# Optimization experiments

Hardware: AMD Instinct MI355X
Metric: run time of the kernel (lower is better)

Reference implementation:

```python
import jax, jax.numpy as jnp
import numpy as np

# Model config (matches init_kwargs)
L_F, DELTA_F, L_S, DELTA_S = 1, 1, 32, 16
HIDDEN = 32       # SSM state dim H
GRU_H = 64        # slow-branch GRU hidden
N_GRU = 4
B, T = 4, 32768


def setup_inputs() -> dict:
    key = jax.random.key(0)
    ks = jax.random.split(key, 13)
    def nrm(k, shape, s=0.05):
        return jax.random.normal(k, shape, dtype=jnp.float32) * s
    return {
        "x": jax.random.normal(ks[0], (B, T), dtype=jnp.float32),
        # SlowBranch params
        "fc_in_w": nrm(ks[1], (GRU_H, 1), 0.3),
        "fc_in_b": nrm(ks[2], (GRU_H,)),
        "gru_wih": nrm(ks[3], (N_GRU, 3 * GRU_H, GRU_H), 0.1),
        "gru_whh": nrm(ks[4], (N_GRU, 3 * GRU_H, GRU_H), 0.1),
        "gru_bih": nrm(ks[5], (N_GRU, 3 * GRU_H)),
        "gru_bhh": nrm(ks[6], (N_GRU, 3 * GRU_H)),
        "out_fc_w": nrm(ks[7], (2 * HIDDEN, GRU_H), 0.1),
        "out_fc_b": nrm(ks[8], (2 * HIDDEN,)),
        # Fast branch params (F_IN: 1->H, F_OUT: H->1)
        "fin_w": nrm(ks[9], (HIDDEN, 1), 0.3),
        "fin_b": nrm(ks[10], (HIDDEN,)),
        "fout_w": nrm(ks[11], (1, HIDDEN), 0.1),
        "fout_b": nrm(ks[12], (1,)),
    }


def _gru_layer(xs, Wih, Whh, bih, bhh):
    """Torch-convention GRU layer. xs: (N, L, H_in) -> (N, L, H)."""
    H = Whh.shape[1]
    # Precompute input-side gate pre-activations: (N, L, 3H)
    xp = jnp.einsum('nlh,gh->nlg', xs, Wih) + bih
    def step(h, xt):
        gh = h @ Whh.T + bhh                       # (N, 3H)
        ir, iz, inew = jnp.split(xt, 3, axis=-1)
        hr, hz, hnew = jnp.split(gh, 3, axis=-1)
        r = jax.nn.sigmoid(ir + hr)
        z = jax.nn.sigmoid(iz + hz)
        n = jnp.tanh(inew + r * hnew)
        h = (1.0 - z) * n + z * h
        return h, h
    h0 = jnp.zeros((xs.shape[0], H), xs.dtype)
    _, ys = jax.lax.scan(step, h0, jnp.swapaxes(xp, 0, 1))  # (L, N, H)
    return jnp.swapaxes(ys, 0, 1)


def reference(x, fc_in_w, fc_in_b, gru_wih, gru_whh, gru_bih, gru_bhh,
              out_fc_w, out_fc_b, fin_w, fin_b, fout_w, fout_b):
    Bsz, Tlen = x.shape
    num_slow = (Tlen - L_S) // DELTA_S + 1

    frame_idx = jnp.arange(num_slow)[:, None] * DELTA_S + jnp.arange(L_S)[None, :]
    x_s = x[:, frame_idx].reshape(Bsz * num_slow, L_S, 1)      # (N, L_s, 1)
    h = jax.nn.relu(x_s * fc_in_w[:, 0] + fc_in_b)             # (N, L_s, GRU_H)
    for l in range(gru_wih.shape[0]):
        h = _gru_layer(h, gru_wih[l], gru_whh[l], gru_bih[l], gru_bhh[l])
    eps = h[:, -1, :] @ out_fc_w.T + out_fc_b                  # (N, 2H)
    eps = eps.reshape(Bsz, num_slow, 2 * HIDDEN)
    A_slow = jax.nn.sigmoid(eps[..., :HIDDEN])                 # (B, S, H)
    g_slow = eps[..., HIDDEN:]                                 # (B, S, H)

    # ---- Fast branch: per-sample diagonal linear SSM scan ----
    delta = DELTA_S // DELTA_F
    idx = jnp.clip(jnp.arange(Tlen) // delta - 1, 0, num_slow - 1)  # (T,)
    A_t = A_slow[:, idx, :]                                    # (B, T, H)
    u_t = (x[..., None] * fin_w[:, 0] + fin_b) * g_slow[:, idx, :]  # (B, T, H)

    def step(hc, inp):
        A, u = inp
        hn = A * hc + u
        return hn, hn
    h0 = jnp.zeros((Bsz, HIDDEN), x.dtype)
    _, h_all = jax.lax.scan(step, h0,
                            (jnp.swapaxes(A_t, 0, 1), jnp.swapaxes(u_t, 0, 1)))
    # h_all: (T, B, H); F_OUT applied to every state
    return jnp.einsum('tbh,h->bt', h_all, fout_w[0]) + fout_b[0]   # (B, T)
```

## Files before the change

kernel.cpp:

```cpp
#include <hip/hip_runtime.h>
#include <hip/hip_bf16.h>

typedef __bf16 bf16x8 __attribute__((ext_vector_type(8)));
typedef short short8 __attribute__((ext_vector_type(8)));
typedef float f32x4 __attribute__((ext_vector_type(4)));
typedef unsigned short ushort_t;

#define T_LEN 32768
#define B_SZ 4
#define NSLOW 2047
#define NSEQ (B_SZ * NSLOW)
#define GH 64
#define G3 192
#define NL 4
#define HID 32
#define NCH 256
#define L2E 1.44269504088896341f

#define OFF_X    0
#define OFF_FCW  131072
#define OFF_FCB  131136
#define OFF_WIH  131200
#define OFF_WHH  180352
#define OFF_BIH  229504
#define OFF_BHH  230272
#define OFF_OFW  231040
#define OFF_OFB  235136
#define OFF_FINW 235200
#define OFF_FINB 235232
#define OFF_FOW  235264
#define OFF_FOB  235296
#define CONV_TOTAL 235297
#define CONV_PAD_BYTES 470656

static __device__ __forceinline__ float bf2f(ushort_t u) {
    union { unsigned u; float f; } c; c.u = ((unsigned)u) << 16; return c.f;
}
static __device__ __forceinline__ ushort_t f2bf(float f) {
    union { float f; unsigned u; } c; c.f = f;
    unsigned r = (c.u + 0x7FFFu + ((c.u >> 16) & 1u)) >> 16;
    return (ushort_t)r;
}
static __device__ __forceinline__ unsigned pk2bf(float a, float b) {
    float2 f; f.x = a; f.y = b;
    __hip_bfloat162 h = __float22bfloat162_rn(f);
    unsigned u;
    __builtin_memcpy(&u, &h, 4);
    return u;
}
static __device__ __forceinline__ f32x4 mfma16(short8 a, short8 b, f32x4 c) {
    return __builtin_amdgcn_mfma_f32_16x16x32_bf16(
        __builtin_bit_cast(bf16x8, a), __builtin_bit_cast(bf16x8, b), c, 0, 0, 0);
}
static __device__ __forceinline__ int xoff(int t, int kb, int seq) {
    return ((((t << 3) + kb) << 4) + (seq ^ (kb & 7))) << 3;
}
static __device__ __forceinline__ short8 load_frag_scaled(const ushort_t* p, float s) {
    uint4 r = *(const uint4*)p;
    unsigned aa[4] = {r.x, r.y, r.z, r.w};
    short8 o;
#pragma unroll
    for (int i = 0; i < 4; ++i) {
        o[2 * i]     = (short)f2bf(bf2f((ushort_t)(aa[i] & 0xffffu)) * s);
        o[2 * i + 1] = (short)f2bf(bf2f((ushort_t)(aa[i] >> 16)) * s);
    }
    return o;
}

struct Ptrs13 { const void* p[13]; };

__global__ __launch_bounds__(256) void convert_kernel(Ptrs13 ptrs,
                                                      int* __restrict__ flag,
                                                      ushort_t* __restrict__ dst)
{
    __shared__ int scnt;
    if (threadIdx.x == 0) scnt = 0;
    __syncthreads();
    {
        ushort_t u = ((const ushort_t*)ptrs.p[0])[threadIdx.x];
        int e = (u >> 7) & 0xFF;
        int ok = (e >= 80 && e <= 141) ? 1 : 0;
#pragma unroll
        for (int d = 1; d < 64; d <<= 1) ok += __shfl_xor(ok, d, 64);
        if ((threadIdx.x & 63) == 0) atomicAdd(&scnt, ok);
    }
    __syncthreads();
    const bool isbf = (scnt >= 224);
    if (blockIdx.x == 0 && threadIdx.x == 0) *flag = isbf ? 1 : 0;

    const int offs[14] = {OFF_X, OFF_FCW, OFF_FCB, OFF_WIH, OFF_WHH, OFF_BIH,
                          OFF_BHH, OFF_OFW, OFF_OFB, OFF_FINW, OFF_FINB,
                          OFF_FOW, OFF_FOB, CONV_TOTAL};
    for (int idx = blockIdx.x * 256 + threadIdx.x; idx < CONV_TOTAL;
         idx += gridDim.x * 256) {
        int s = 0;
#pragma unroll
        for (int j = 1; j < 13; ++j) if (idx >= offs[j]) s = j;
        int k = idx - offs[s];
        ushort_t v = isbf ? ((const ushort_t*)ptrs.p[s])[k]
                          : f2bf(((const float*)ptrs.p[s])[k]);
        dst[idx] = v;
    }
}

__global__ __launch_bounds__(256, 2) void gru_kernel(
    const ushort_t* __restrict__ x, const ushort_t* __restrict__ fcw,
    const ushort_t* __restrict__ fcb, const ushort_t* __restrict__ wih,
    const ushort_t* __restrict__ whh, const ushort_t* __restrict__ bih,
    const ushort_t* __restrict__ bhh, const ushort_t* __restrict__ ofw,
    const ushort_t* __restrict__ ofb, float* __restrict__ Aslow,
    float* __restrict__ gslow)
{
    __shared__ short8 Xs8[4096];
    short* Xs = (short*)Xs8;
    const int tid = threadIdx.x;
    const int w = tid >> 6, lane = tid & 63;
    const int q = lane >> 4, m = lane & 15;
    const int jb = w * 16;
    const int n0 = blockIdx.x * 16;

#pragma unroll 1
    for (int ii = 0; ii < 16; ++ii) {
        int cid = ii * 256 + tid;
        int seq = cid & 15, kb = (cid >> 4) & 7, t = cid >> 7;
        int n = n0 + seq; if (n > NSEQ - 1) n = NSEQ - 1;
        int b = n / NSLOW, s = n - b * NSLOW;
        float xv = bf2f(x[b * T_LEN + s * 16 + t]);
        short8 v;
#pragma unroll
        for (int i = 0; i < 8; ++i) {
            int g = kb * 8 + i;
            float h = fmaf(xv, bf2f(fcw[g]), bf2f(fcb[g]));
            h = h > 0.f ? h : 0.f;
            v[i] = (short)f2bf(h);
        }
        Xs8[xoff(t, kb, seq) >> 3] = v;
    }

    const int col0 = jb + 4 * q;
    const int kbw = (col0 >> 3);
    const int wsub = (col0 & 7);
    const int kofs = q * 8;
    const int wbase0 = ((kbw << 4) + (m ^ (kbw & 7))) * 8 + wsub;

    float hc[4];
#pragma unroll 1
    for (int l = 0; l < NL; ++l) {
        const ushort_t* wl = wih + l * G3 * GH;
        const ushort_t* ul = whh + l * G3 * GH;
        short8 wR0 = load_frag_scaled(wl + (0 * 64 + jb + m) * 64 + kofs, -L2E);
        short8 wR1 = load_frag_scaled(wl + (0 * 64 + jb + m) * 64 + 32 + kofs, -L2E);
        short8 wZ0 = load_frag_scaled(wl + (1 * 64 + jb + m) * 64 + kofs, -L2E);
        short8 wZ1 = load_frag_scaled(wl + (1 * 64 + jb + m) * 64 + 32 + kofs, -L2E);
        short8 wN0 = load_frag_scaled(wl + (2 * 64 + jb + m) * 64 + kofs, 2.f * L2E);
        short8 wN1 = load_frag_scaled(wl + (2 * 64 + jb + m) * 64 + 32 + kofs, 2.f * L2E);
        short8 uR0 = load_frag_scaled(ul + (0 * 64 + jb + m) * 64 + kofs, -L2E);
        short8 uR1 = load_frag_scaled(ul + (0 * 64 + jb + m) * 64 + 32 + kofs, -L2E);
        short8 uZ0 = load_frag_scaled(ul + (1 * 64 + jb + m) * 64 + kofs, -L2E);
        short8 uZ1 = load_frag_scaled(ul + (1 * 64 + jb + m) * 64 + 32 + kofs, -L2E);
        short8 uN0 = load_frag_scaled(ul + (2 * 64 + jb + m) * 64 + kofs, 2.f * L2E);
        short8 uN1 = load_frag_scaled(ul + (2 * 64 + jb + m) * 64 + 32 + kofs, 2.f * L2E);

        f32x4 bRv, bZv, bNXv, bNHv;
#pragma unroll
        for (int i = 0; i < 4; ++i) {
            int c = col0 + i;
            bRv[i]  = -L2E * (bf2f(bih[l * G3 + c]) + bf2f(bhh[l * G3 + c]));
            bZv[i]  = -L2E * (bf2f(bih[l * G3 + 64 + c]) + bf2f(bhh[l * G3 + 64 + c]));
            bNXv[i] = 2.f * L2E * bf2f(bih[l * G3 + 128 + c]);
            bNHv[i] = 2.f * L2E * bf2f(bhh[l * G3 + 128 + c]);
        }

        hc[0] = hc[1] = hc[2] = hc[3] = 0.f;

        __syncthreads();
        int iA = xoff(0, q, m) >> 3;
        int iB = xoff(0, 4 + q, m) >> 3;
        int wb = wbase0;

        short8 cx0 = Xs8[iA], cx1 = Xs8[iB];
        short8 nx0 = Xs8[iA + 128], nx1 = Xs8[iB + 128];
        f32x4 xR = bRv, xZ = bZv, xN = bNXv;
        xR = mfma16(wR0, cx0, xR); xR = mfma16(wR1, cx1, xR);
        xZ = mfma16(wZ0, cx0, xZ); xZ = mfma16(wZ1, cx1, xZ);
        xN = mfma16(wN0, cx0, xN); xN = mfma16(wN1, cx1, xN);
#pragma unroll
        for (int i = 0; i < 4; ++i) {
            float r = __builtin_amdgcn_rcpf(1.f + __builtin_amdgcn_exp2f(xR[i]));
            float z = __builtin_amdgcn_rcpf(1.f + __builtin_amdgcn_exp2f(xZ[i]));
            float yp = fmaf(r, bNHv[i], xN[i]);
            float nn = fmaf(-2.f,
                __builtin_amdgcn_rcpf(1.f + __builtin_amdgcn_exp2f(yp)), 1.f);
            hc[i] = fmaf(z, hc[i] - nn, nn);
        }
        *(uint2*)(Xs + wb) = make_uint2(pk2bf(hc[0], hc[1]), pk2bf(hc[2], hc[3]));
        xR = bRv; xZ = bZv; xN = bNXv;
        xR = mfma16(wR0, nx0, xR); xR = mfma16(wR1, nx1, xR);
        xZ = mfma16(wZ0, nx0, xZ); xZ = mfma16(wZ1, nx1, xZ);
        xN = mfma16(wN0, nx0, xN); xN = mfma16(wN1, nx1, xN);
        iA += 128; iB += 128; wb += 1024;

#pragma unroll 1
        for (int t = 1; t < 32; ++t) {
            __syncthreads();
            short8 bh0 = Xs8[iA - 128];
            short8 bh1 = Xs8[iB - 128];
            short8 px0, px1;
            if (t < 31) {
                px0 = Xs8[iA + 128];
                px1 = Xs8[iB + 128];
            }
            f32x4 aR = xR, aZ = xZ, aNH = bNHv;
            aR  = mfma16(uR0, bh0, aR);  aR  = mfma16(uR1, bh1, aR);
            aZ  = mfma16(uZ0, bh0, aZ);  aZ  = mfma16(uZ1, bh1, aZ);
            aNH = mfma16(uN0, bh0, aNH); aNH = mfma16(uN1, bh1, aNH);
#pragma unroll
            for (int i = 0; i < 4; ++i) {
                float r = __builtin_amdgcn_rcpf(1.f + __builtin_amdgcn_exp2f(aR[i]));
                float z = __builtin_amdgcn_rcpf(1.f + __builtin_amdgcn_exp2f(aZ[i]));
                float yp = fmaf(r, aNH[i], xN[i]);
                float nn = fmaf(-2.f,
                    __builtin_amdgcn_rcpf(1.f + __builtin_amdgcn_exp2f(yp)), 1.f);
                hc[i] = fmaf(z, hc[i] - nn, nn);
            }
            *(uint2*)(Xs + wb) =
                make_uint2(pk2bf(hc[0], hc[1]), pk2bf(hc[2], hc[3]));
            if (t < 31) {
                xR = bRv; xZ = bZv; xN = bNXv;
                xR = mfma16(wR0, px0, xR); xR = mfma16(wR1, px1, xR);
                xZ = mfma16(wZ0, px0, xZ); xZ = mfma16(wZ1, px1, xZ);
                xN = mfma16(wN0, px0, xN); xN = mfma16(wN1, px1, xN);
            }
            iA += 128; iB += 128; wb += 1024;
        }
    }

    __syncthreads();
    short8 aL0 = Xs8[xoff(31, q, m) >> 3];
    short8 aL1 = Xs8[xoff(31, 4 + q, m) >> 3];
    float sc = (w < 2) ? -L2E : 1.f;
    short8 o0 = load_frag_scaled(ofw + (jb + m) * 64 + kofs, sc);
    short8 o1 = load_frag_scaled(ofw + (jb + m) * 64 + 32 + kofs, sc);
    f32x4 aE = {bf2f(ofb[col0]) * sc, bf2f(ofb[col0 + 1]) * sc,
                bf2f(ofb[col0 + 2]) * sc, bf2f(ofb[col0 + 3]) * sc};
    aE = mfma16(o0, aL0, aE);
    aE = mfma16(o1, aL1, aE);
    int n = n0 + m;
    if (w < 2) {
        f32x4 v;
#pragma unroll
        for (int i = 0; i < 4; ++i)
            v[i] = __builtin_amdgcn_rcpf(1.f + __builtin_amdgcn_exp2f(aE[i]));
        *(f32x4*)(Aslow + n * HID + col0) = v;
    } else {
        *(f32x4*)(gslow + n * HID + (col0 - 32)) = aE;
    }
}

__global__ __launch_bounds__(256) void pass1_kernel(
    const ushort_t* __restrict__ x, const float* __restrict__ Aslow,
    const float* __restrict__ gslow, const ushort_t* __restrict__ finw,
    const ushort_t* __restrict__ finb, float* __restrict__ P,
    float* __restrict__ S)
{
    int gt = blockIdx.x * 256 + threadIdx.x;
    int h = gt & 31, c = (gt >> 5) & 255, b = gt >> 13;
    float fw = bf2f(finw[h]), fb = bf2f(finb[h]);
    float Pv = 1.f, Sv = 0.f;
    int t0 = c * 128;
#pragma unroll 1
    for (int seg = 0; seg < 8; ++seg) {
        int sidx = (t0 >> 4) + seg - 1;
        if (sidx < 0) sidx = 0;
        if (sidx > NSLOW - 1) sidx = NSLOW - 1;
        float A = Aslow[(b * NSLOW + sidx) * HID + h];
        float g = gslow[(b * NSLOW + sidx) * HID + h];
        float fwg = fw * g, fbg = fb * g;
        const uint4* px = (const uint4*)(x + b * T_LEN + t0 + seg * 16);
        uint4 ra = px[0], rb = px[1];
        unsigned xa[8] = {ra.x, ra.y, ra.z, ra.w, rb.x, rb.y, rb.z, rb.w};
#pragma unroll
        for (int j = 0; j < 8; ++j) {
            float x0 = bf2f((ushort_t)(xa[j] & 0xffffu));
            float x1 = bf2f((ushort_t)(xa[j] >> 16));
            Sv = fmaf(A, Sv, fmaf(x0, fwg, fbg));
            Sv = fmaf(A, Sv, fmaf(x1, fwg, fbg));
        }
        float A2 = A * A, A4 = A2 * A2, A8 = A4 * A4;
        Pv *= A8 * A8;
    }
    P[(b * HID + h) * NCH + c] = Pv;
    S[(b * HID + h) * NCH + c] = Sv;
}

__global__ __launch_bounds__(128) void scan_kernel(
    const float* __restrict__ P, const float* __restrict__ S,
    float* __restrict__ Hpre)
{
    int tid = threadIdx.x;
    const float4* p4 = (const float4*)(P + tid * NCH);
    const float4* s4 = (const float4*)(S + tid * NCH);
    float* hp = Hpre + tid * NCH;
    float hr = 0.f;
#pragma unroll 8
    for (int c = 0; c < NCH / 4; ++c) {
        float4 pv = p4[c], sv = s4[c];
        hp[4 * c + 0] = hr; hr = fmaf(pv.x, hr, sv.x);
        hp[4 * c + 1] = hr; hr = fmaf(pv.y, hr, sv.y);
        hp[4 * c + 2] = hr; hr = fmaf(pv.z, hr, sv.z);
        hp[4 * c + 3] = hr; hr = fmaf(pv.w, hr, sv.w);
    }
}

__global__ __launch_bounds__(256) void pass2_kernel(
    const ushort_t* __restrict__ x, const float* __restrict__ Aslow,
    const float* __restrict__ gslow, const float* __restrict__ Hpre,
    const ushort_t* __restrict__ finw, const ushort_t* __restrict__ finb,
    const ushort_t* __restrict__ fow, const ushort_t* __restrict__ fob,
    const int* __restrict__ flag, void* __restrict__ outv)
{
    int wv = blockIdx.x * 4 + (threadIdx.x >> 6);
    int lane = threadIdx.x & 63;
    int half = lane >> 5, h = lane & 31;
    int pair = wv * 2 + half;
    int b = pair >> 8, c = pair & 255;
    const bool isbf = (*flag != 0);
    ushort_t* outb = (ushort_t*)outv;
    float* outf = (float*)outv;
    float hv = Hpre[(b * HID + h) * NCH + c];
    float fw = bf2f(finw[h]), fb = bf2f(finb[h]);
    float wo = bf2f(fow[h]), ob = bf2f(fob[0]);
    int t0 = c * 128;
#pragma unroll 1
    for (int blk = 0; blk < 4; ++blk) {
        float ykeep = 0.f;
        float A = 0.f, fwg = 0.f, fbg = 0.f;
#pragma unroll
        for (int tt = 0; tt < 32; ++tt) {
            int t = t0 + blk * 32 + tt;
            if ((tt & 15) == 0) {
                int sidx = (t >> 4) - 1;
                if (sidx < 0) sidx = 0;
                A = Aslow[(b * NSLOW + sidx) * HID + h];
                float g = gslow[(b * NSLOW + sidx) * HID + h];
                fwg = fw * g; fbg = fb * g;
            }
            float xv = bf2f(x[b * T_LEN + t]);
            hv = fmaf(A, hv, fmaf(xv, fwg, fbg));
            float y = hv * wo;
            y += __shfl_xor(y, 1, 64);
            y += __shfl_xor(y, 2, 64);
            y += __shfl_xor(y, 4, 64);
            y += __shfl_xor(y, 8, 64);
            y += __shfl_xor(y, 16, 64);
            if (tt == h) ykeep = y + ob;
        }
        int oidx = b * T_LEN + t0 + blk * 32 + h;
        if (isbf) outb[oidx] = f2bf(ykeep);
        else      outf[oidx] = ykeep;
    }
}

extern "C" void kernel_launch(void* const* d_in, const int* in_sizes, int n_in,
                              void* d_out, int out_size, void* d_ws, size_t ws_size,
                              hipStream_t stream)
{
    ushort_t* cv = (ushort_t*)d_ws;
    const ushort_t* x    = cv + OFF_X;
    const ushort_t* fcw  = cv + OFF_FCW;
    const ushort_t* fcb  = cv + OFF_FCB;
    const ushort_t* wih  = cv + OFF_WIH;
    const ushort_t* whh  = cv + OFF_WHH;
    const ushort_t* bih  = cv + OFF_BIH;
    const ushort_t* bhh  = cv + OFF_BHH;
    const ushort_t* ofw  = cv + OFF_OFW;
    const ushort_t* ofb  = cv + OFF_OFB;
    const ushort_t* finw = cv + OFF_FINW;
    const ushort_t* finb = cv + OFF_FINB;
    const ushort_t* fow  = cv + OFF_FOW;
    const ushort_t* fob  = cv + OFF_FOB;

    float* Aslow = (float*)((char*)d_ws + CONV_PAD_BYTES);
    float* gslow = Aslow + 8192 * 32;
    float* P     = gslow + 8192 * 32;
    float* S     = P + 4 * 32 * NCH;
    float* Hpre  = S + 4 * 32 * NCH;
    int*   flag  = (int*)(Hpre + 4 * 32 * NCH);

    Ptrs13 ptrs;
    for (int i = 0; i < 13; ++i) ptrs.p[i] = d_in[i];

    convert_kernel<<<dim3(920), dim3(256), 0, stream>>>(ptrs, flag, cv);
    gru_kernel<<<dim3(512), dim3(256), 0, stream>>>(
        x, fcw, fcb, wih, whh, bih, bhh, ofw, ofb, Aslow, gslow);
    pass1_kernel<<<dim3(128), dim3(256), 0, stream>>>(
        x, Aslow, gslow, finw, finb, P, S);
    scan_kernel<<<dim3(1), dim3(128), 0, stream>>>(P, S, Hpre);
    pass2_kernel<<<dim3(128), dim3(256), 0, stream>>>(
        x, Aslow, gslow, Hpre, finw, finb, fow, fob, flag, d_out);
}
```

Measured before the change: 191.4 us.

## Drop conversion kernel and fuse fast-path passes with grid-wide sync

Removes the separate dtype-conversion kernel; the GRU and fast-path kernels now detect bf16 per wave and read raw inputs directly. The pass1, scan and pass2 kernels merge into one kernel: the last block to finish runs the chunk scan and releases the others through an atomic flag. This removes three launches and the bf16 staging copy. In exchange it relies on all 128 blocks being co-resident for the spin-wait, and repeats the dtype check inside every kernel.

```diff
diff --git a/kernel.cpp b/kernel.cpp
--- a/kernel.cpp
+++ b/kernel.cpp
@@ -17,22 +17,6 @@
 #define NCH 256
 #define L2E 1.44269504088896341f
 
-#define OFF_X    0
-#define OFF_FCW  131072
-#define OFF_FCB  131136
-#define OFF_WIH  131200
-#define OFF_WHH  180352
-#define OFF_BIH  229504
-#define OFF_BHH  230272
-#define OFF_OFW  231040
-#define OFF_OFB  235136
-#define OFF_FINW 235200
-#define OFF_FINB 235232
-#define OFF_FOW  235264
-#define OFF_FOB  235296
-#define CONV_TOTAL 235297
-#define CONV_PAD_BYTES 470656
-
 static __device__ __forceinline__ float bf2f(ushort_t u) {
     union { unsigned u; float f; } c; c.u = ((unsigned)u) << 16; return c.f;
 }
@@ -55,61 +39,53 @@
 static __device__ __forceinline__ int xoff(int t, int kb, int seq) {
     return ((((t << 3) + kb) << 4) + (seq ^ (kb & 7))) << 3;
 }
-static __device__ __forceinline__ short8 load_frag_scaled(const ushort_t* p, float s) {
-    uint4 r = *(const uint4*)p;
-    unsigned aa[4] = {r.x, r.y, r.z, r.w};
+
+static __device__ __forceinline__ bool detect_bf16(const void* xin) {
+    const ushort_t* xb = (const ushort_t*)xin;
+    int lane = threadIdx.x & 63;
+    int cnt = 0;
+#pragma unroll
+    for (int i = 0; i < 4; ++i) {
+        ushort_t u = xb[lane * 4 + i];
+        int e = (u >> 7) & 0xFF;
+        cnt += (e >= 80 && e <= 141) ? 1 : 0;
+    }
+#pragma unroll
+    for (int d = 1; d < 64; d <<= 1) cnt += __shfl_xor(cnt, d, 64);
+    return cnt >= 224;
+}
+static __device__ __forceinline__ float ldf(const void* p, bool isbf, int idx) {
+    return isbf ? bf2f(((const ushort_t*)p)[idx]) : ((const float*)p)[idx];
+}
+static __device__ __forceinline__ short8 load_frag(const void* base, bool isbf,
+                                                   int off, float s) {
     short8 o;
-#pragma unroll
-    for (int i = 0; i < 4; ++i) {
-        o[2 * i]     = (short)f2bf(bf2f((ushort_t)(aa[i] & 0xffffu)) * s);
-        o[2 * i + 1] = (short)f2bf(bf2f((ushort_t)(aa[i] >> 16)) * s);
+    if (isbf) {
+        uint4 r = *(const uint4*)((const ushort_t*)base + off);
+        unsigned aa[4] = {r.x, r.y, r.z, r.w};
+#pragma unroll
+        for (int i = 0; i < 4; ++i) {
+            o[2 * i]     = (short)f2bf(bf2f((ushort_t)(aa[i] & 0xffffu)) * s);
+            o[2 * i + 1] = (short)f2bf(bf2f((ushort_t)(aa[i] >> 16)) * s);
+        }
+    } else {
+        const float4* p = (const float4*)((const float*)base + off);
+        float4 a = p[0], b = p[1];
+        o[0] = (short)f2bf(a.x * s); o[1] = (short)f2bf(a.y * s);
+        o[2] = (short)f2bf(a.z * s); o[3] = (short)f2bf(a.w * s);
+        o[4] = (short)f2bf(b.x * s); o[5] = (short)f2bf(b.y * s);
+        o[6] = (short)f2bf(b.z * s); o[7] = (short)f2bf(b.w * s);
     }
     return o;
 }
 
-struct Ptrs13 { const void* p[13]; };
-
-__global__ __launch_bounds__(256) void convert_kernel(Ptrs13 ptrs,
-                                                      int* __restrict__ flag,
-                                                      ushort_t* __restrict__ dst)
-{
-    __shared__ int scnt;
-    if (threadIdx.x == 0) scnt = 0;
-    __syncthreads();
-    {
-        ushort_t u = ((const ushort_t*)ptrs.p[0])[threadIdx.x];
-        int e = (u >> 7) & 0xFF;
-        int ok = (e >= 80 && e <= 141) ? 1 : 0;
-#pragma unroll
-        for (int d = 1; d < 64; d <<= 1) ok += __shfl_xor(ok, d, 64);
-        if ((threadIdx.x & 63) == 0) atomicAdd(&scnt, ok);
-    }
-    __syncthreads();
-    const bool isbf = (scnt >= 224);
-    if (blockIdx.x == 0 && threadIdx.x == 0) *flag = isbf ? 1 : 0;
-
-    const int offs[14] = {OFF_X, OFF_FCW, OFF_FCB, OFF_WIH, OFF_WHH, OFF_BIH,
-                          OFF_BHH, OFF_OFW, OFF_OFB, OFF_FINW, OFF_FINB,
-                          OFF_FOW, OFF_FOB, CONV_TOTAL};
-    for (int idx = blockIdx.x * 256 + threadIdx.x; idx < CONV_TOTAL;
-         idx += gridDim.x * 256) {
-        int s = 0;
-#pragma unroll
-        for (int j = 1; j < 13; ++j) if (idx >= offs[j]) s = j;
-        int k = idx - offs[s];
-        ushort_t v = isbf ? ((const ushort_t*)ptrs.p[s])[k]
-                          : f2bf(((const float*)ptrs.p[s])[k]);
-        dst[idx] = v;
-    }
-}
-
 __global__ __launch_bounds__(256, 2) void gru_kernel(
-    const ushort_t* __restrict__ x, const ushort_t* __restrict__ fcw,
-    const ushort_t* __restrict__ fcb, const ushort_t* __restrict__ wih,
-    const ushort_t* __restrict__ whh, const ushort_t* __restrict__ bih,
-    const ushort_t* __restrict__ bhh, const ushort_t* __restrict__ ofw,
-    const ushort_t* __restrict__ ofb, float* __restrict__ Aslow,
-    float* __restrict__ gslow)
+    const void* __restrict__ xin, const void* __restrict__ fcw,
+    const void* __restrict__ fcb, const void* __restrict__ wih,
+    const void* __restrict__ whh, const void* __restrict__ bih,
+    const void* __restrict__ bhh, const void* __restrict__ ofw,
+    const void* __restrict__ ofb, float* __restrict__ Aslow,
+    float* __restrict__ gslow, int* __restrict__ sync)
 {
     __shared__ short8 Xs8[4096];
     short* Xs = (short*)Xs8;
@@ -119,18 +95,22 @@
     const int jb = w * 16;
     const int n0 = blockIdx.x * 16;
 
+    if (blockIdx.x == 0 && tid == 0) { sync[0] = 0; sync[1] = 0; }
+
+    const bool isbf = detect_bf16(xin);
+
 #pragma unroll 1
     for (int ii = 0; ii < 16; ++ii) {
         int cid = ii * 256 + tid;
         int seq = cid & 15, kb = (cid >> 4) & 7, t = cid >> 7;
         int n = n0 + seq; if (n > NSEQ - 1) n = NSEQ - 1;
         int b = n / NSLOW, s = n - b * NSLOW;
-        float xv = bf2f(x[b * T_LEN + s * 16 + t]);
+        float xv = ldf(xin, isbf, b * T_LEN + s * 16 + t);
         short8 v;
 #pragma unroll
         for (int i = 0; i < 8; ++i) {
             int g = kb * 8 + i;
-            float h = fmaf(xv, bf2f(fcw[g]), bf2f(fcb[g]));
+            float h = fmaf(xv, ldf(fcw, isbf, g), ldf(fcb, isbf, g));
             h = h > 0.f ? h : 0.f;
             v[i] = (short)f2bf(h);
         }
@@ -146,29 +126,28 @@
     float hc[4];
 #pragma unroll 1
     for (int l = 0; l < NL; ++l) {
-        const ushort_t* wl = wih + l * G3 * GH;
-        const ushort_t* ul = whh + l * G3 * GH;
-        short8 wR0 = load_frag_scaled(wl + (0 * 64 + jb + m) * 64 + kofs, -L2E);
-        short8 wR1 = load_frag_scaled(wl + (0 * 64 + jb + m) * 64 + 32 + kofs, -L2E);
-        short8 wZ0 = load_frag_scaled(wl + (1 * 64 + jb + m) * 64 + kofs, -L2E);
-        short8 wZ1 = load_frag_scaled(wl + (1 * 64 + jb + m) * 64 + 32 + kofs, -L2E);
-        short8 wN0 = load_frag_scaled(wl + (2 * 64 + jb + m) * 64 + kofs, 2.f * L2E);
-        short8 wN1 = load_frag_scaled(wl + (2 * 64 + jb + m) * 64 + 32 + kofs, 2.f * L2E);
-        short8 uR0 = load_frag_scaled(ul + (0 * 64 + jb + m) * 64 + kofs, -L2E);
-        short8 uR1 = load_frag_scaled(ul + (0 * 64 + jb + m) * 64 + 32 + kofs, -L2E);
-        short8 uZ0 = load_frag_scaled(ul + (1 * 64 + jb + m) * 64 + kofs, -L2E);
-        short8 uZ1 = load_frag_scaled(ul + (1 * 64 + jb + m) * 64 + 32 + kofs, -L2E);
-        short8 uN0 = load_frag_scaled(ul + (2 * 64 + jb + m) * 64 + kofs, 2.f * L2E);
-        short8 uN1 = load_frag_scaled(ul + (2 * 64 + jb + m) * 64 + 32 + kofs, 2.f * L2E);
+        const int wl = l * G3 * GH;
+        short8 wR0 = load_frag(wih, isbf, wl + (0 * 64 + jb + m) * 64 + kofs, -L2E);
+        short8 wR1 = load_frag(wih, isbf, wl + (0 * 64 + jb + m) * 64 + 32 + kofs, -L2E);
+        short8 wZ0 = load_frag(wih, isbf, wl + (1 * 64 + jb + m) * 64 + kofs, -L2E);
+        short8 wZ1 = load_frag(wih, isbf, wl + (1 * 64 + jb + m) * 64 + 32 + kofs, -L2E);
+        short8 wN0 = load_frag(wih, isbf, wl + (2 * 64 + jb + m) * 64 + kofs, 2.f * L2E);
+        short8 wN1 = load_frag(wih, isbf, wl + (2 * 64 + jb + m) * 64 + 32 + kofs, 2.f * L2E);
+        short8 uR0 = load_frag(whh, isbf, wl + (0 * 64 + jb + m) * 64 + kofs, -L2E);
+        short8 uR1 = load_frag(whh, isbf, wl + (0 * 64 + jb + m) * 64 + 32 + kofs, -L2E);
+        short8 uZ0 = load_frag(whh, isbf, wl + (1 * 64 + jb + m) * 64 + kofs, -L2E);
+        short8 uZ1 = load_frag(whh, isbf, wl + (1 * 64 + jb + m) * 64 + 32 + kofs, -L2E);
+        short8 uN0 = load_frag(whh, isbf, wl + (2 * 64 + jb + m) * 64 + kofs, 2.f * L2E);
+        short8 uN1 = load_frag(whh, isbf, wl + (2 * 64 + jb + m) * 64 + 32 + kofs, 2.f * L2E);
 
         f32x4 bRv, bZv, bNXv, bNHv;
 #pragma unroll
         for (int i = 0; i < 4; ++i) {
             int c = col0 + i;
-            bRv[i]  = -L2E * (bf2f(bih[l * G3 + c]) + bf2f(bhh[l * G3 + c]));
-            bZv[i]  = -L2E * (bf2f(bih[l * G3 + 64 + c]) + bf2f(bhh[l * G3 + 64 + c]));
-            bNXv[i] = 2.f * L2E * bf2f(bih[l * G3 + 128 + c]);
-            bNHv[i] = 2.f * L2E * bf2f(bhh[l * G3 + 128 + c]);
+            bRv[i]  = -L2E * (ldf(bih, isbf, l * G3 + c) + ldf(bhh, isbf, l * G3 + c));
+            bZv[i]  = -L2E * (ldf(bih, isbf, l * G3 + 64 + c) + ldf(bhh, isbf, l * G3 + 64 + c));
+            bNXv[i] = 2.f * L2E * ldf(bih, isbf, l * G3 + 128 + c);
+            bNHv[i] = 2.f * L2E * ldf(bhh, isbf, l * G3 + 128 + c);
         }
 
         hc[0] = hc[1] = hc[2] = hc[3] = 0.f;
@@ -239,10 +218,10 @@
     short8 aL0 = Xs8[xoff(31, q, m) >> 3];
     short8 aL1 = Xs8[xoff(31, 4 + q, m) >> 3];
     float sc = (w < 2) ? -L2E : 1.f;
-    short8 o0 = load_frag_scaled(ofw + (jb + m) * 64 + kofs, sc);
-    short8 o1 = load_frag_scaled(ofw + (jb + m) * 64 + 32 + kofs, sc);
-    f32x4 aE = {bf2f(ofb[col0]) * sc, bf2f(ofb[col0 + 1]) * sc,
-                bf2f(ofb[col0 + 2]) * sc, bf2f(ofb[col0 + 3]) * sc};
+    short8 o0 = load_frag(ofw, isbf, (jb + m) * 64 + kofs, sc);
+    short8 o1 = load_frag(ofw, isbf, (jb + m) * 64 + 32 + kofs, sc);
+    f32x4 aE = {ldf(ofb, isbf, col0) * sc, ldf(ofb, isbf, col0 + 1) * sc,
+                ldf(ofb, isbf, col0 + 2) * sc, ldf(ofb, isbf, col0 + 3) * sc};
     aE = mfma16(o0, aL0, aE);
     aE = mfma16(o1, aL1, aE);
     int n = n0 + m;
@@ -257,79 +236,110 @@
     }
 }
 
-__global__ __launch_bounds__(256) void pass1_kernel(
-    const ushort_t* __restrict__ x, const float* __restrict__ Aslow,
-    const float* __restrict__ gslow, const ushort_t* __restrict__ finw,
-    const ushort_t* __restrict__ finb, float* __restrict__ P,
-    float* __restrict__ S)
+__global__ __launch_bounds__(256) void fastpath_kernel(
+    const void* __restrict__ xin, const float* __restrict__ Aslow,
+    const float* __restrict__ gslow, const void* __restrict__ finw,
+    const void* __restrict__ finb, const void* __restrict__ fow,
+    const void* __restrict__ fob, float* __restrict__ P,
+    float* __restrict__ S, float* __restrict__ Hpre,
+    int* __restrict__ sync, void* __restrict__ outv)
 {
-    int gt = blockIdx.x * 256 + threadIdx.x;
-    int h = gt & 31, c = (gt >> 5) & 255, b = gt >> 13;
-    float fw = bf2f(finw[h]), fb = bf2f(finb[h]);
-    float Pv = 1.f, Sv = 0.f;
-    int t0 = c * 128;
+    const bool isbf = detect_bf16(xin);
+    const int tid = threadIdx.x;
+
+    {
+        int gt = blockIdx.x * 256 + tid;
+        int h = gt & 31, c = (gt >> 5) & 255, b = gt >> 13;
+        float fw = ldf(finw, isbf, h), fb = ldf(finb, isbf, h);
+        float Pv = 1.f, Sv = 0.f;
+        int t0 = c * 128;
 #pragma unroll 1
-    for (int seg = 0; seg < 8; ++seg) {
-        int sidx = (t0 >> 4) + seg - 1;
-        if (sidx < 0) sidx = 0;
-        if (sidx > NSLOW - 1) sidx = NSLOW - 1;
-        float A = Aslow[(b * NSLOW + sidx) * HID + h];
-        float g = gslow[(b * NSLOW + sidx) * HID + h];
-        float fwg = fw * g, fbg = fb * g;
-        const uint4* px = (const uint4*)(x + b * T_LEN + t0 + seg * 16);
-        uint4 ra = px[0], rb = px[1];
-        unsigned xa[8] = {ra.x, ra.y, ra.z, ra.w, rb.x, rb.y, rb.z, rb.w};
-#pragma unroll
-        for (int j = 0; j < 8; ++j) {
-            float x0 = bf2f((ushort_t)(xa[j] & 0xffffu));
-            float x1 = bf2f((ushort_t)(xa[j] >> 16));
-            Sv = fmaf(A, Sv, fmaf(x0, fwg, fbg));
-            Sv = fmaf(A, Sv, fmaf(x1, fwg, fbg));
-        }
-        float A2 = A * A, A4 = A2 * A2, A8 = A4 * A4;
-        Pv *= A8 * A8;
-    }
-    P[(b * HID + h) * NCH + c] = Pv;
-    S[(b * HID + h) * NCH + c] = Sv;
-}
-
-__global__ __launch_bounds__(128) void scan_kernel(
-    const float* __restrict__ P, const float* __restrict__ S,
-    float* __restrict__ Hpre)
-{
-    int tid = threadIdx.x;
-    const float4* p4 = (const float4*)(P + tid * NCH);
-    const float4* s4 = (const float4*)(S + tid * NCH);
-    float* hp = Hpre + tid * NCH;
-    float hr = 0.f;
+        for (int seg = 0; seg < 8; ++seg) {
+            int sidx = (t0 >> 4) + seg - 1;
+            if (sidx < 0) sidx = 0;
+            if (sidx > NSLOW - 1) sidx = NSLOW - 1;
+            float A = Aslow[(b * NSLOW + sidx) * HID + h];
+            float g = gslow[(b * NSLOW + sidx) * HID + h];
+            float fwg = fw * g, fbg = fb * g;
+            float xs[16];
+            if (isbf) {
+                const uint4* px = (const uint4*)((const ushort_t*)xin +
+                                                 b * T_LEN + t0 + seg * 16);
+                uint4 ra = px[0], rb = px[1];
+                unsigned xa[8] = {ra.x, ra.y, ra.z, ra.w, rb.x, rb.y, rb.z, rb.w};
+#pragma unroll
+                for (int j = 0; j < 8; ++j) {
+                    xs[2 * j]     = bf2f((ushort_t)(xa[j] & 0xffffu));
+                    xs[2 * j + 1] = bf2f((ushort_t)(xa[j] >> 16));
+                }
+            } else {
+                const float4* px = (const float4*)((const float*)xin +
+                                                   b * T_LEN + t0 + seg * 16);
+#pragma unroll
+                for (int j = 0; j < 4; ++j) {
+                    float4 v = px[j];
+                    xs[4 * j] = v.x; xs[4 * j + 1] = v.y;
+                    xs[4 * j + 2] = v.z; xs[4 * j + 3] = v.w;
+                }
+            }
+#pragma unroll
+            for (int j = 0; j < 16; ++j)
+                Sv = fmaf(A, Sv, fmaf(xs[j], fwg, fbg));
+            float A2 = A * A, A4 = A2 * A2, A8 = A4 * A4;
+            Pv *= A8 * A8;
+        }
+        P[(b * HID + h) * NCH + c] = Pv;
+        S[(b * HID + h) * NCH + c] = Sv;
+    }
+
+    __threadfence();
+    __syncthreads();
+    __shared__ int sLast;
+    if (tid == 0) {
+        int old = atomicAdd(sync, 1);
+        sLast = (old == gridDim.x - 1) ? 1 : 0;
+    }
+    __syncthreads();
+    if (sLast) {
+        __threadfence();
+        if (tid < 128) {
+            const float4* p4 = (const float4*)(P + tid * NCH);
+            const float4* s4 = (const float4*)(S + tid * NCH);
+            float* hp = Hpre + tid * NCH;
+            float hr = 0.f;
 #pragma unroll 8
-    for (int c = 0; c < NCH / 4; ++c) {
-        float4 pv = p4[c], sv = s4[c];
-        hp[4 * c + 0] = hr; hr = fmaf(pv.x, hr, sv.x);
-        hp[4 * c + 1] = hr; hr = fmaf(pv.y, hr, sv.y);
-        hp[4 * c + 2] = hr; hr = fmaf(pv.z, hr, sv.z);
-        hp[4 * c + 3] = hr; hr = fmaf(pv.w, hr, sv.w);
-    }
-}
-
-__global__ __launch_bounds__(256) void pass2_kernel(
-    const ushort_t* __restrict__ x, const float* __restrict__ Aslow,
-    const float* __restrict__ gslow, const float* __restrict__ Hpre,
-    const ushort_t* __restrict__ finw, const ushort_t* __restrict__ finb,
-    const ushort_t* __restrict__ fow, const ushort_t* __restrict__ fob,
-    const int* __restrict__ flag, void* __restrict__ outv)
-{
-    int wv = blockIdx.x * 4 + (threadIdx.x >> 6);
-    int lane = threadIdx.x & 63;
+            for (int c = 0; c < NCH / 4; ++c) {
+                float4 pv = p4[c], sv = s4[c];
+                hp[4 * c + 0] = hr; hr = fmaf(pv.x, hr, sv.x);
+                hp[4 * c + 1] = hr; hr = fmaf(pv.y, hr, sv.y);
+                hp[4 * c + 2] = hr; hr = fmaf(pv.z, hr, sv.z);
+                hp[4 * c + 3] = hr; hr = fmaf(pv.w, hr, sv.w);
+            }
+        }
+        __syncthreads();
+        if (tid == 0) {
+            __threadfence();
+            __hip_atomic_store(sync + 1, 1, __ATOMIC_RELEASE,
+                               __HIP_MEMORY_SCOPE_AGENT);
+        }
+    }
+    if (tid == 0) {
+        while (__hip_atomic_load(sync + 1, __ATOMIC_ACQUIRE,
+                                 __HIP_MEMORY_SCOPE_AGENT) == 0)
+            __builtin_amdgcn_s_sleep(16);
+    }
+    __syncthreads();
+
+    int wv = blockIdx.x * 4 + (tid >> 6);
+    int lane = tid & 63;
     int half = lane >> 5, h = lane & 31;
     int pair = wv * 2 + half;
     int b = pair >> 8, c = pair & 255;
-    const bool isbf = (*flag != 0);
     ushort_t* outb = (ushort_t*)outv;
     float* outf = (float*)outv;
     float hv = Hpre[(b * HID + h) * NCH + c];
-    float fw = bf2f(finw[h]), fb = bf2f(finb[h]);
-    float wo = bf2f(fow[h]), ob = bf2f(fob[0]);
+    float fw = ldf(finw, isbf, h), fb = ldf(finb, isbf, h);
+    float wo = ldf(fow, isbf, h), ob = ldf(fob, isbf, 0);
     int t0 = c * 128;
 #pragma unroll 1
     for (int blk = 0; blk < 4; ++blk) {
@@ -345,7 +355,7 @@
                 float g = gslow[(b * NSLOW + sidx) * HID + h];
                 fwg = fw * g; fbg = fb * g;
             }
-            float xv = bf2f(x[b * T_LEN + t]);
+            float xv = ldf(xin, isbf, b * T_LEN + t);
             hv = fmaf(A, hv, fmaf(xv, fwg, fbg));
             float y = hv * wo;
             y += __shfl_xor(y, 1, 64);
@@ -365,37 +375,29 @@
                               void* d_out, int out_size, void* d_ws, size_t ws_size,
                               hipStream_t stream)
 {
-    ushort_t* cv = (ushort_t*)d_ws;
-    const ushort_t* x    = cv + OFF_X;
-    const ushort_t* fcw  = cv + OFF_FCW;
-    const ushort_t* fcb  = cv + OFF_FCB;
-    const ushort_t* wih  = cv + OFF_WIH;
-    const ushort_t* whh  = cv + OFF_WHH;
-    const ushort_t* bih  = cv + OFF_BIH;
-    const ushort_t* bhh  = cv + OFF_BHH;
-    const ushort_t* ofw  = cv + OFF_OFW;
-    const ushort_t* ofb  = cv + OFF_OFB;
-    const ushort_t* finw = cv + OFF_FINW;
-    const ushort_t* finb = cv + OFF_FINB;
-    const ushort_t* fow  = cv + OFF_FOW;
-    const ushort_t* fob  = cv + OFF_FOB;
-
-    float* Aslow = (float*)((char*)d_ws + CONV_PAD_BYTES);
+    const void* xin  = d_in[0];
+    const void* fcw  = d_in[1];
+    const void* fcb  = d_in[2];
+    const void* wih  = d_in[3];
+    const void* whh  = d_in[4];
+    const void* bih  = d_in[5];
+    const void* bhh  = d_in[6];
+    const void* ofw  = d_in[7];
+    const void* ofb  = d_in[8];
+    const void* finw = d_in[9];
+    const void* finb = d_in[10];
+    const void* fow  = d_in[11];
+    const void* fob  = d_in[12];
+
+    float* Aslow = (float*)d_ws;
     float* gslow = Aslow + 8192 * 32;
     float* P     = gslow + 8192 * 32;
     float* S     = P + 4 * 32 * NCH;
     float* Hpre  = S + 4 * 32 * NCH;
-    int*   flag  = (int*)(Hpre + 4 * 32 * NCH);
-
-    Ptrs13 ptrs;
-    for (int i = 0; i < 13; ++i) ptrs.p[i] = d_in[i];
-
-    convert_kernel<<<dim3(920), dim3(256), 0, stream>>>(ptrs, flag, cv);
+    int*   sync  = (int*)(Hpre + 4 * 32 * NCH);
+
     gru_kernel<<<dim3(512), dim3(256), 0, stream>>>(
-        x, fcw, fcb, wih, whh, bih, bhh, ofw, ofb, Aslow, gslow);
-    pass1_kernel<<<dim3(128), dim3(256), 0, stream>>>(
-        x, Aslow, gslow, finw, finb, P, S);
-    scan_kernel<<<dim3(1), dim3(128), 0, stream>>>(P, S, Hpre);
-    pass2_kernel<<<dim3(128), dim3(256), 0, stream>>>(
-        x, Aslow, gslow, Hpre, finw, finb, fow, fob, flag, d_out);
-}
+        xin, fcw, fcb, wih, whh, bih, bhh, ofw, ofb, Aslow, gslow, sync);
+    fastpath_kernel<<<dim3(128), dim3(256), 0, stream>>>(
+        xin, Aslow, gslow, finw, finb, fow, fob, P, S, Hpre, sync, d_out);
+}
```

Result: slower. 268.3 us (+40.1%).
